# Kernel tuning notes

Hardware: AMD Instinct MI355X
Metric: run time of the kernel (lower is better)

The kernel has to match this reference:

```python
import jax, jax.numpy as jnp
import numpy as np

V, E, H2, B, T, OUT = 50000, 300, 512, 32, 512, 256
H = H2 // 2  # hidden per direction


def _rand_mask(key, lengths, n_true):
    # exactly n_true True positions per row, all within the valid prefix [0, len)
    t = jnp.arange(T)[None, :]
    r = jax.random.uniform(key, (B, T)) + (t >= lengths[:, None]) * 10.0
    idx = jnp.argsort(r, axis=1)[:, :n_true]
    mask = jnp.zeros((B, T), dtype=bool)
    return mask.at[jnp.arange(B)[:, None], idx].set(True)


def setup_inputs() -> dict:
    key = jax.random.key(0)
    ks = jax.random.split(key, 12)
    inputs = jax.random.randint(ks[0], (B, T), 0, V)
    lengths = jnp.sort(jax.random.randint(ks[1], (B,), OUT, T + 1))[::-1]
    lengths = lengths.at[0].set(T)  # max length == padded length
    fmask = _rand_mask(ks[2], lengths, OUT)
    bmask = _rand_mask(ks[3], lengths, OUT)
    emb_scale = np.sqrt(3.0 / E).astype(np.float32)
    emb = jax.random.uniform(ks[4], (V, E), minval=-emb_scale, maxval=emb_scale, dtype=jnp.float32)
    k = 1.0 / np.sqrt(H).astype(np.float32)
    def u(kk, shape):
        return jax.random.uniform(kk, shape, minval=-k, maxval=k, dtype=jnp.float32)
    return {
        'inputs': inputs, 'seq_length': lengths, 'fmask': fmask, 'bmask': bmask,
        'out_seq_length': OUT, 'emb': emb,
        'W_ih_f': u(ks[5], (4 * H, E)), 'W_hh_f': u(ks[6], (4 * H, H)),
        'b_ih_f': u(ks[7], (4 * H,)), 'b_hh_f': u(ks[8], (4 * H,)),
        'W_ih_b': u(ks[9], (4 * H, E)), 'W_hh_b': u(ks[10], (4 * H, H)),
        'b_ih_b': u(ks[11], (4 * H,)), 'b_hh_b': u(ks[7], (4 * H,)),
    }


def run_lstm(xe, W_ih, W_hh, b_ih, b_hh):
    # PyTorch LSTM cell, gate order i,f,g,o. xe: (B,T,E) -> (B,T,H)
    xg = jnp.einsum('bte,ge->btg', xe, W_ih) + (b_ih + b_hh)
    def step(carry, xg_t):
        h, c = carry
        g = xg_t + h @ W_hh.T
        i, f, gg, o = jnp.split(g, 4, axis=-1)
        c = jax.nn.sigmoid(f) * c + jax.nn.sigmoid(i) * jnp.tanh(gg)
        h = jax.nn.sigmoid(o) * jnp.tanh(c)
        return (h, c), h
    h0 = jnp.zeros((xe.shape[0], W_hh.shape[1]), xe.dtype)
    _, hs = jax.lax.scan(step, (h0, h0), xg.transpose(1, 0, 2))
    return hs.transpose(1, 0, 2)


def select_masked(x, mask, out_len):
    # masked_select row-major order == indices of True in increasing t
    idx = jnp.argsort(jnp.logical_not(mask), axis=1, stable=True)[:, :out_len]
    return jnp.take_along_axis(x, idx[:, :, None], axis=1)


def reference(inputs, seq_length, fmask, bmask, out_seq_length, emb,
              W_ih_f, W_hh_f, b_ih_f, b_hh_f, W_ih_b, W_hh_b, b_ih_b, b_hh_b):
    t = jnp.arange(inputs.shape[1])[None, :]          # (1,T)
    valid = t < seq_length[:, None]                   # (B,T)
    # forward direction (dropout is identity at inference)
    f_out = run_lstm(emb[inputs], W_ih_f, W_hh_f, b_ih_f, b_hh_f)
    f_out = f_out * valid[..., None]                  # pad_packed zeros beyond len
    fsel = select_masked(f_out, fmask, out_seq_length)
    # per-batch sequence reversal of valid prefix (padding stays in place)
    rev_idx = jnp.where(valid, seq_length[:, None] - 1 - t, t)
    rinputs = jnp.take_along_axis(inputs, rev_idx, axis=1)
    b_out = run_lstm(emb[rinputs], W_ih_b, W_hh_b, b_ih_b, b_hh_b)
    b_out = b_out * valid[..., None]
    bsel = select_masked(b_out, bmask, out_seq_length)
    # re-reverse selected backward outputs per batch
    k = jnp.minimum(seq_length, out_seq_length)[:, None]
    t2 = jnp.arange(out_seq_length)[None, :]
    idx2 = jnp.where(t2 < k, out_seq_length - 1 - t2, t2 - k)
    bsel = jnp.take_along_axis(bsel, idx2[:, :, None], axis=1)
    return jnp.concatenate([fsel, bsel], axis=2)      # (B,out_seq,2H)
```

## Files before the change

### kernel.cpp

```cpp
#include <hip/hip_runtime.h>
#include <hip/hip_bf16.h>

#define B_   32
#define T_   512
#define E_   300
#define H_   256
#define OUT_ 256
#define ECH  100
#define GROWP 293

typedef unsigned long long u64;

__global__ __launch_bounds__(64) void slots_kernel(
    const unsigned char* __restrict__ fm, const unsigned char* __restrict__ bm,
    int* __restrict__ fslot, int* __restrict__ bpos)
{
    __shared__ unsigned char fL[B_ * T_];
    __shared__ unsigned char bL[B_ * T_];
    const int tid = threadIdx.x;

    const unsigned int* fw = (const unsigned int*)fm;
    int cnt = 0;
    for (int i = tid; i < 128; i += 64) {
        unsigned int v = fw[i];
        cnt += ((v & 0xFFu) != 0) + ((v & 0xFF00u) != 0)
             + ((v & 0xFF0000u) != 0) + ((v >> 24) != 0);
    }
#pragma unroll
    for (int off = 32; off; off >>= 1) cnt += __shfl_down(cnt, off, 64);
    bool isbool = __shfl(cnt, 0, 64) > 128;

    if (isbool) {
        for (int i = tid; i < B_ * T_ / 4; i += 64) {
            ((unsigned int*)fL)[i] = ((const unsigned int*)fm)[i];
            ((unsigned int*)bL)[i] = ((const unsigned int*)bm)[i];
        }
    } else {
        const unsigned int* bw = (const unsigned int*)bm;
        for (int i = tid; i < B_ * T_; i += 64) {
            fL[i] = fw[i] != 0;
            bL[i] = bw[i] != 0;
        }
    }
    __syncthreads();

    if (tid < B_) {
        int jf = 0, jb = 0;
        for (int t = 0; t < T_; ++t) {
            bool f = fL[tid * T_ + t] != 0;
            bool g = bL[tid * T_ + t] != 0;
            fslot[tid * T_ + t] = f ? (jf++) : -1;
            bpos [tid * T_ + t] = g ? (OUT_ - 1 - (jb++)) : -1;
        }
    }
}

__global__ __launch_bounds__(256) void xg_gemm(
    const int* __restrict__ inputs, const int* __restrict__ seqlen,
    const float* __restrict__ emb,
    const float* __restrict__ Wihf, const float* __restrict__ Wihb,
    const float* __restrict__ bihf, const float* __restrict__ bhhf,
    const float* __restrict__ bihb, const float* __restrict__ bhhb,
    float* __restrict__ xg, int t0, int TcMax)
{
    const int tg   = blockIdx.y;
    const int dir  = blockIdx.z;
    const int rblk = blockIdx.x * 64;
    const int tid  = threadIdx.x;

    __shared__ float eL[4][B_][ECH];
    __shared__ int   tokS[4][B_];

    if (tid < 128) {
        int t4 = tid >> 5, b = tid & 31;
        int t = t0 + tg * 4 + t4;
        int L = seqlen[b];
        int tt = t;
        if (dir) tt = (t < L) ? (L - 1 - t) : t;
        tokS[t4][b] = inputs[b * T_ + tt];
    }

    const float* W = dir ? Wihb : Wihf;
    const int b  = tid & 31;
    const int r8 = tid >> 5;

    float acc[4][8];
#pragma unroll
    for (int t4 = 0; t4 < 4; ++t4)
#pragma unroll
        for (int m = 0; m < 8; ++m) acc[t4][m] = 0.f;

    for (int ec = 0; ec < 3; ++ec) {
        __syncthreads();
        for (int idx = tid; idx < 3200; idx += 256) {
            int q  = idx % 25;
            int bb = (idx / 25) & 31;
            int t4 = idx / (25 * 32);
            const float* erow = emb + (size_t)tokS[t4][bb] * E_ + ec * ECH;
            *(float4*)&eL[t4][bb][q * 4] = *(const float4*)(erow + q * 4);
        }
        __syncthreads();

        for (int e4 = 0; e4 < 25; ++e4) {
            float4 w4[8];
#pragma unroll
            for (int m = 0; m < 8; ++m)
                w4[m] = *(const float4*)(W + (size_t)(rblk + r8 + m * 8) * E_
                                         + ec * ECH + e4 * 4);
#pragma unroll
            for (int t4 = 0; t4 < 4; ++t4) {
                float4 h4 = *(const float4*)&eL[t4][b][e4 * 4];
#pragma unroll
                for (int m = 0; m < 8; ++m)
                    acc[t4][m] += h4.x * w4[m].x + h4.y * w4[m].y
                                + h4.z * w4[m].z + h4.w * w4[m].w;
            }
        }
    }

    const float* bi = dir ? bihb : bihf;
    const float* bh = dir ? bhhb : bhhf;
#pragma unroll
    for (int t4 = 0; t4 < 4; ++t4) {
        float* outp = xg + (size_t)(dir * TcMax + tg * 4 + t4) * (1024 * B_);
#pragma unroll
        for (int m = 0; m < 8; ++m) {
            int row = rblk + r8 + m * 8;
            outp[(size_t)row * B_ + b] = acc[t4][m] + bi[row] + bh[row];
        }
    }
}

__global__ __launch_bounds__(512, 2) void fused_lstm(
    const int* __restrict__ inputs, const int* __restrict__ seqlen,
    const float* __restrict__ emb,
    const float* __restrict__ Wihf, const float* __restrict__ Whhf,
    const float* __restrict__ bihf, const float* __restrict__ bhhf,
    const float* __restrict__ Wihb, const float* __restrict__ Whhb,
    const float* __restrict__ bihb, const float* __restrict__ bhhb,
    const int* __restrict__ fslot, const int* __restrict__ bpos,
    float* __restrict__ hbuf, float* __restrict__ cbuf,
    int* __restrict__ barr, int* __restrict__ xgcnt,
    float* __restrict__ xg, float* __restrict__ out,
    int t0, int Tc, int fused)
{
    const int wg  = blockIdx.x;
    const int tid = threadIdx.x;
    __shared__ __align__(16) float smem[13824];

    if (wg >= 128) {
        float* eL   = smem;
        int*   tokS = (int*)(smem + 12800);
        const int hw = wg - 128;

        for (int j = hw; j < 2048; j += 128) {
            const int tg  = j >> 4;
            const int dir = (j >> 3) & 1;
            const int rp  = j & 7;
            const int rblk = (rp * 2 + (tid >> 8)) * 64;

            if (tid < 128) {
                int t4 = tid >> 5, b = tid & 31;
                int t = tg * 4 + t4;
                int L = seqlen[b];
                int tt = t;
                if (dir) tt = (t < L) ? (L - 1 - t) : t;
                tokS[t4 * B_ + b] = inputs[b * T_ + tt];
            }

            const float* W  = dir ? Wihb : Wihf;
            const int ltid = tid & 255;
            const int b  = ltid & 31;
            const int r8 = ltid >> 5;

            float acc[4][8];
#pragma unroll
            for (int t4 = 0; t4 < 4; ++t4)
#pragma unroll
                for (int m = 0; m < 8; ++m) acc[t4][m] = 0.f;

            for (int ec = 0; ec < 3; ++ec) {
                __syncthreads();
                for (int idx = tid; idx < 3200; idx += 512) {
                    int q  = idx % 25;
                    int bb = (idx / 25) & 31;
                    int t4 = idx / (25 * 32);
                    const float* erow = emb + (size_t)tokS[t4 * B_ + bb] * E_ + ec * ECH;
                    *(float4*)&eL[(t4 * B_ + bb) * ECH + q * 4] = *(const float4*)(erow + q * 4);
                }
                __syncthreads();

                for (int e4 = 0; e4 < 25; ++e4) {
                    float4 w4[8];
#pragma unroll
                    for (int m = 0; m < 8; ++m)
                        w4[m] = *(const float4*)(W + (size_t)(rblk + r8 + m * 8) * E_
                                                 + ec * ECH + e4 * 4);
#pragma unroll
                    for (int t4 = 0; t4 < 4; ++t4) {
                        float4 h4 = *(const float4*)&eL[(t4 * B_ + b) * ECH + e4 * 4];
#pragma unroll
                        for (int m = 0; m < 8; ++m)
                            acc[t4][m] += h4.x * w4[m].x + h4.y * w4[m].y
                                        + h4.z * w4[m].z + h4.w * w4[m].w;
                    }
                }
            }

            const float* bi = dir ? bihb : bihf;
            const float* bh = dir ? bhhb : bhhf;
#pragma unroll
            for (int t4 = 0; t4 < 4; ++t4) {
                float* outp = xg + (size_t)(dir * 512 + tg * 4 + t4) * (1024 * B_);
#pragma unroll
                for (int m = 0; m < 8; ++m) {
                    int row = rblk + r8 + m * 8;
                    __hip_atomic_store(&outp[(size_t)row * B_ + b],
                                       acc[t4][m] + bi[row] + bh[row],
                                       __ATOMIC_RELAXED, __HIP_MEMORY_SCOPE_AGENT);
                }
            }
            __syncthreads();
            if (tid == 0)
                __hip_atomic_fetch_add(&xgcnt[dir * 128 + tg], 1,
                                       __ATOMIC_RELAXED, __HIP_MEMORY_SCOPE_AGENT);
        }
        return;
    }

    float* hP   = smem;
    float* gbuf = smem + 8704;
    int*   sL   = (int*)(smem + 8704 + 4688);

    const int dir = wg >> 6;
    const int wgd = wg & 63;
    const int u0  = wgd * 4;

    const int rg  = tid & 3;
    const int bgr = (tid >> 2) & 7;
    const int kq  = tid >> 5;

    const float* Whh = dir ? Whhb : Whhf;

    float w[4][16];
#pragma unroll
    for (int r = 0; r < 4; ++r) {
        const float* wr = Whh + (size_t)(rg * H_ + u0 + r) * H_ + kq * 16;
#pragma unroll
        for (int q = 0; q < 4; ++q) {
            float4 v = *(const float4*)(wr + q * 4);
            w[r][q * 4 + 0] = v.x; w[r][q * 4 + 1] = v.y;
            w[r][q * 4 + 2] = v.z; w[r][q * 4 + 3] = v.w;
        }
    }
    if (tid < B_) sL[tid] = seqlen[tid];
    __syncthreads();

    const int ul = (tid >> 5) & 3, bb = tid & 31;
    float c_reg = 0.f;
    if (t0 > 0 && tid < 128)
        c_reg = cbuf[(size_t)(dir * 64 + wgd) * 128 + ul * 32 + bb];

    if (fused) {
        if (tid == 0) {
            const int* xc = xgcnt + dir * 128 + (t0 >> 2);
            while (__hip_atomic_load(xc, __ATOMIC_RELAXED,
                                     __HIP_MEMORY_SCOPE_AGENT) < 8)
                __builtin_amdgcn_s_sleep(1);
        }
        __syncthreads();
    }
    float xgv0 = 0.f, xgv1 = 0.f, xgv2 = 0.f, xgv3 = 0.f;
    if (tid < 128) {
        const float* xp = xg + (size_t)(dir * Tc) * 32768 + (u0 + ul) * 32 + bb;
        xgv0 = __hip_atomic_load(xp, __ATOMIC_RELAXED, __HIP_MEMORY_SCOPE_AGENT);
        xgv1 = __hip_atomic_load(xp + 256 * 32, __ATOMIC_RELAXED, __HIP_MEMORY_SCOPE_AGENT);
        xgv2 = __hip_atomic_load(xp + 512 * 32, __ATOMIC_RELAXED, __HIP_MEMORY_SCOPE_AGENT);
        xgv3 = __hip_atomic_load(xp + 768 * 32, __ATOMIC_RELAXED, __HIP_MEMORY_SCOPE_AGENT);
    }

    int* myflag = barr + dir * 64 + wgd;

    for (int tc = 0; tc < Tc; ++tc) {
        const int t = t0 + tc;

        if (tc > 0) {
            if (tid < 64) {
                const int* fp = barr + dir * 64 + tid;
                const int gneed = (fused && tc + 1 < Tc) ? ((t0 + tc + 1) >> 2) : -1;
                const int* xc = xgcnt + dir * 128 + (gneed < 0 ? 0 : gneed);
                for (;;) {
                    bool ok = __hip_atomic_load(fp, __ATOMIC_RELAXED,
                                                __HIP_MEMORY_SCOPE_AGENT) >= tc;
                    if (gneed >= 0 && tid == 0)
                        ok = ok && (__hip_atomic_load(xc, __ATOMIC_RELAXED,
                                                      __HIP_MEMORY_SCOPE_AGENT) >= 8);
                    if (__all(ok)) break;
                    __builtin_amdgcn_s_sleep(1);
                }
            }
            __syncthreads();
        }

        float xgn0 = 0.f, xgn1 = 0.f, xgn2 = 0.f, xgn3 = 0.f;
        if (tc + 1 < Tc && tid < 128) {
            const float* xp = xg + (size_t)(dir * Tc + tc + 1) * 32768 + (u0 + ul) * 32 + bb;
            xgn0 = __hip_atomic_load(xp, __ATOMIC_RELAXED, __HIP_MEMORY_SCOPE_AGENT);
            xgn1 = __hip_atomic_load(xp + 256 * 32, __ATOMIC_RELAXED, __HIP_MEMORY_SCOPE_AGENT);
            xgn2 = __hip_atomic_load(xp + 512 * 32, __ATOMIC_RELAXED, __HIP_MEMORY_SCOPE_AGENT);
            xgn3 = __hip_atomic_load(xp + 768 * 32, __ATOMIC_RELAXED, __HIP_MEMORY_SCOPE_AGENT);
        }

        u64 hr[8];
        if (t > 0) {
            const u64* hp64 = (const u64*)(hbuf +
                (size_t)(dir * 2 + ((t - 1) & 1)) * (64 * 32 * 4));
#pragma unroll
            for (int i = 0; i < 8; ++i)
                hr[i] = __hip_atomic_load(hp64 + tid + 512 * i, __ATOMIC_RELAXED,
                                          __HIP_MEMORY_SCOPE_AGENT);
#pragma unroll
            for (int i = 0; i < 8; ++i) {
                int g = tid + 512 * i;
                int f4 = g >> 1, jp = g & 1;
                int k4 = f4 >> 5, b = f4 & 31;
                int base = ((k4 >> 2) * 8 + (b >> 2)) * 68 + (k4 & 3) * 16 + (b & 3);
                union { u64 u; float f[2]; } cv; cv.u = hr[i];
                hP[base + 8 * jp]     = cv.f[0];
                hP[base + 8 * jp + 4] = cv.f[1];
            }
        }
        __syncthreads();

        float acc[4][4];
#pragma unroll
        for (int r = 0; r < 4; ++r)
#pragma unroll
            for (int bi = 0; bi < 4; ++bi) acc[r][bi] = 0.f;

        if (t > 0) {
            const float* hblk = &hP[(kq * 8 + bgr) * 68];
#pragma unroll
            for (int kk = 0; kk < 16; ++kk) {
                float4 h4 = *(const float4*)(hblk + kk * 4);
#pragma unroll
                for (int r = 0; r < 4; ++r) {
                    acc[r][0] += w[r][kk] * h4.x;
                    acc[r][1] += w[r][kk] * h4.y;
                    acc[r][2] += w[r][kk] * h4.z;
                    acc[r][3] += w[r][kk] * h4.w;
                }
            }
        }

#pragma unroll
        for (int r = 0; r < 4; ++r)
#pragma unroll
            for (int bi = 0; bi < 4; ++bi)
                acc[r][bi] += __shfl_xor(acc[r][bi], 32, 64);

        if (((tid >> 5) & 1) == 0) {
            const int kq2 = kq >> 1;
#pragma unroll
            for (int r = 0; r < 4; ++r)
#pragma unroll
                for (int bi = 0; bi < 4; ++bi)
                    gbuf[(r * 4 + rg) * GROWP + (bgr * 4 + bi) * 9 + kq2] = acc[r][bi];
        }
        __syncthreads();

        if (tid < 128) {
            const int u = u0 + ul;
            float hnew;
            if (t < sL[bb]) {
                float gi = xgv0, gf = xgv1, gg = xgv2, go = xgv3;
#pragma unroll
                for (int q = 0; q < 8; ++q) {
                    gi += gbuf[(ul * 4 + 0) * GROWP + bb * 9 + q];
                    gf += gbuf[(ul * 4 + 1) * GROWP + bb * 9 + q];
                    gg += gbuf[(ul * 4 + 2) * GROWP + bb * 9 + q];
                    go += gbuf[(ul * 4 + 3) * GROWP + bb * 9 + q];
                }
                float si = 1.f / (1.f + expf(-gi));
                float sf = 1.f / (1.f + expf(-gf));
                float so = 1.f / (1.f + expf(-go));
                c_reg = sf * c_reg + si * tanhf(gg);
                hnew  = so * tanhf(c_reg);
                if (dir == 0) {
                    int j = fslot[bb * T_ + t];
                    if (j >= 0)
                        __hip_atomic_store(&out[((size_t)bb * OUT_ + j) * 512 + u],
                                           hnew, __ATOMIC_RELAXED,
                                           __HIP_MEMORY_SCOPE_AGENT);
                } else {
                    int p = bpos[bb * T_ + t];
                    if (p >= 0)
                        __hip_atomic_store(&out[((size_t)bb * OUT_ + p) * 512 + 256 + u],
                                           hnew, __ATOMIC_RELAXED,
                                           __HIP_MEMORY_SCOPE_AGENT);
                }
            } else {
                hnew = hP[((u >> 4) * 8 + (bb >> 2)) * 68 + (u & 15) * 4 + (bb & 3)];
            }
            float* hn = hbuf + (size_t)(dir * 2 + (t & 1)) * (64 * 32 * 4);
            __hip_atomic_store(&hn[(wgd * 32 + bb) * 4 + ul], hnew,
                               __ATOMIC_RELAXED, __HIP_MEMORY_SCOPE_AGENT);
        }
        xgv0 = xgn0; xgv1 = xgn1; xgv2 = xgn2; xgv3 = xgn3;
        __syncthreads();

        if (tc + 1 < Tc && tid == 0)
            __hip_atomic_store(myflag, tc + 1, __ATOMIC_RELAXED,
                               __HIP_MEMORY_SCOPE_AGENT);
    }

    if (tid < 128)
        cbuf[(size_t)(dir * 64 + wgd) * 128 + ul * 32 + bb] = c_reg;
}

extern "C" void kernel_launch(void* const* d_in, const int* in_sizes, int n_in,
                              void* d_out, int out_size, void* d_ws, size_t ws_size,
                              hipStream_t stream) {
    const int*           inputs = (const int*)d_in[0];
    const int*           seqlen = (const int*)d_in[1];
    const unsigned char* fm     = (const unsigned char*)d_in[2];
    const unsigned char* bm     = (const unsigned char*)d_in[3];
    const float* emb  = (const float*)d_in[5];
    const float* Wihf = (const float*)d_in[6];
    const float* Whhf = (const float*)d_in[7];
    const float* bihf = (const float*)d_in[8];
    const float* bhhf = (const float*)d_in[9];
    const float* Wihb = (const float*)d_in[10];
    const float* Whhb = (const float*)d_in[11];
    const float* bihb = (const float*)d_in[12];
    const float* bhhb = (const float*)d_in[13];
    float* out = (float*)d_out;

    char* ws = (char*)d_ws;
    int*   fslot = (int*)(ws);
    int*   bpos  = (int*)(ws + 65536);
    float* hbuf  = (float*)(ws + 131072);
    float* cbuf  = (float*)(ws + 262144);
    int*   barr  = (int*)(ws + 327680);
    int*   xgcnt = (int*)(ws + 328192);
    float* xg    = (float*)(ws + 393216);
    (void)in_sizes; (void)n_in; (void)out_size;

    size_t avail = (ws_size > 393216) ? ws_size - 393216 : 0;
    int Tc = 4;
    for (int c = 512; c >= 4; c >>= 1)
        if ((size_t)c * 262144 <= avail) { Tc = c; break; }

    slots_kernel<<<1, 64, 0, stream>>>(fm, bm, fslot, bpos);

    if (Tc == 512) {
        (void)hipMemsetAsync(barr, 0, 512 + 1024, stream);
        fused_lstm<<<256, 512, 0, stream>>>(
            inputs, seqlen, emb, Wihf, Whhf, bihf, bhhf,
            Wihb, Whhb, bihb, bhhb, fslot, bpos,
            hbuf, cbuf, barr, xgcnt, xg, out, 0, 512, 1);
    } else {
        for (int t0 = 0; t0 < T_; t0 += Tc) {
            dim3 g(16, Tc / 4, 2);
            xg_gemm<<<g, 256, 0, stream>>>(inputs, seqlen, emb, Wihf, Wihb,
                                           bihf, bhhf, bihb, bhhb, xg, t0, Tc);
            (void)hipMemsetAsync(barr, 0, 512 + 1024, stream);
            fused_lstm<<<128, 512, 0, stream>>>(
                inputs, seqlen, emb, Wihf, Whhf, bihf, bhhf,
                Wihb, Whhb, bihb, bhhb, fslot, bpos,
                hbuf, cbuf, barr, xgcnt, xg, out, t0, Tc, 0);
        }
    }
}
```

Measured before the change: 2.087 ms.

## Poll barrier flags in every wave, relayout h exchange, defer output stores

```diff
diff --git a/kernel.cpp b/kernel.cpp
--- a/kernel.cpp
+++ b/kernel.cpp
@@ -239,6 +239,8 @@
     const int rg  = tid & 3;
     const int bgr = (tid >> 2) & 7;
     const int kq  = tid >> 5;
+    const int wv  = tid >> 6;
+    const int lane = tid & 63;
 
     const float* Whh = dir ? Whhb : Whhf;
 
@@ -285,21 +287,18 @@
         const int t = t0 + tc;
 
         if (tc > 0) {
-            if (tid < 64) {
-                const int* fp = barr + dir * 64 + tid;
-                const int gneed = (fused && tc + 1 < Tc) ? ((t0 + tc + 1) >> 2) : -1;
-                const int* xc = xgcnt + dir * 128 + (gneed < 0 ? 0 : gneed);
-                for (;;) {
-                    bool ok = __hip_atomic_load(fp, __ATOMIC_RELAXED,
-                                                __HIP_MEMORY_SCOPE_AGENT) >= tc;
-                    if (gneed >= 0 && tid == 0)
-                        ok = ok && (__hip_atomic_load(xc, __ATOMIC_RELAXED,
-                                                      __HIP_MEMORY_SCOPE_AGENT) >= 8);
-                    if (__all(ok)) break;
-                    __builtin_amdgcn_s_sleep(1);
-                }
-            }
-            __syncthreads();
+            const int* fp = barr + dir * 64 + wv + 8 * (lane & 7);
+            const int gneed = (fused && wv < 2 && tc + 1 < Tc) ? ((t0 + tc + 1) >> 2) : -1;
+            const int* xc = xgcnt + dir * 128 + (gneed < 0 ? 0 : gneed);
+            for (;;) {
+                bool ok = __hip_atomic_load(fp, __ATOMIC_RELAXED,
+                                            __HIP_MEMORY_SCOPE_AGENT) >= tc;
+                if (gneed >= 0)
+                    ok = ok && (__hip_atomic_load(xc, __ATOMIC_RELAXED,
+                                                  __HIP_MEMORY_SCOPE_AGENT) >= 8);
+                if (__all(ok)) break;
+                __builtin_amdgcn_s_sleep(1);
+            }
         }
 
         float xgn0 = 0.f, xgn1 = 0.f, xgn2 = 0.f, xgn3 = 0.f;
@@ -311,23 +310,21 @@
             xgn3 = __hip_atomic_load(xp + 768 * 32, __ATOMIC_RELAXED, __HIP_MEMORY_SCOPE_AGENT);
         }
 
-        u64 hr[8];
         if (t > 0) {
             const u64* hp64 = (const u64*)(hbuf +
-                (size_t)(dir * 2 + ((t - 1) & 1)) * (64 * 32 * 4));
+                (size_t)(dir * 2 + ((t - 1) & 1)) * 8192);
+            u64 hr[8];
 #pragma unroll
             for (int i = 0; i < 8; ++i)
                 hr[i] = __hip_atomic_load(hp64 + tid + 512 * i, __ATOMIC_RELAXED,
                                           __HIP_MEMORY_SCOPE_AGENT);
 #pragma unroll
             for (int i = 0; i < 8; ++i) {
-                int g = tid + 512 * i;
-                int f4 = g >> 1, jp = g & 1;
-                int k4 = f4 >> 5, b = f4 & 31;
-                int base = ((k4 >> 2) * 8 + (b >> 2)) * 68 + (k4 & 3) * 16 + (b & 3);
-                union { u64 u; float f[2]; } cv; cv.u = hr[i];
-                hP[base + 8 * jp]     = cv.f[0];
-                hP[base + 8 * jp + 4] = cv.f[1];
+                int j = tid + 512 * i;
+                int k  = (j >> 6) * 4 + ((j >> 4) & 3);
+                int b0 = (j & 15) * 2;
+                int addr = ((k >> 4) * 8 + (b0 >> 2)) * 68 + (k & 15) * 4 + (b0 & 3);
+                *(u64*)&hP[addr] = hr[i];
             }
         }
         __syncthreads();
@@ -369,9 +366,10 @@
         }
         __syncthreads();
 
+        float hnew = 0.f;
+        float* oaddr = nullptr;
         if (tid < 128) {
             const int u = u0 + ul;
-            float hnew;
             if (t < sL[bb]) {
                 float gi = xgv0, gf = xgv1, gg = xgv2, go = xgv3;
 #pragma unroll
@@ -388,22 +386,16 @@
                 hnew  = so * tanhf(c_reg);
                 if (dir == 0) {
                     int j = fslot[bb * T_ + t];
-                    if (j >= 0)
-                        __hip_atomic_store(&out[((size_t)bb * OUT_ + j) * 512 + u],
-                                           hnew, __ATOMIC_RELAXED,
-                                           __HIP_MEMORY_SCOPE_AGENT);
+                    if (j >= 0) oaddr = &out[((size_t)bb * OUT_ + j) * 512 + u];
                 } else {
                     int p = bpos[bb * T_ + t];
-                    if (p >= 0)
-                        __hip_atomic_store(&out[((size_t)bb * OUT_ + p) * 512 + 256 + u],
-                                           hnew, __ATOMIC_RELAXED,
-                                           __HIP_MEMORY_SCOPE_AGENT);
+                    if (p >= 0) oaddr = &out[((size_t)bb * OUT_ + p) * 512 + 256 + u];
                 }
             } else {
                 hnew = hP[((u >> 4) * 8 + (bb >> 2)) * 68 + (u & 15) * 4 + (bb & 3)];
             }
-            float* hn = hbuf + (size_t)(dir * 2 + (t & 1)) * (64 * 32 * 4);
-            __hip_atomic_store(&hn[(wgd * 32 + bb) * 4 + ul], hnew,
+            float* hn = hbuf + (size_t)(dir * 2 + (t & 1)) * 8192;
+            __hip_atomic_store(&hn[wgd * 128 + tid], hnew,
                                __ATOMIC_RELAXED, __HIP_MEMORY_SCOPE_AGENT);
         }
         xgv0 = xgn0; xgv1 = xgn1; xgv2 = xgn2; xgv3 = xgn3;
@@ -411,6 +403,9 @@
 
         if (tc + 1 < Tc && tid == 0)
             __hip_atomic_store(myflag, tc + 1, __ATOMIC_RELAXED,
+                               __HIP_MEMORY_SCOPE_AGENT);
+        if (oaddr)
+            __hip_atomic_store(oaddr, hnew, __ATOMIC_RELAXED,
                                __HIP_MEMORY_SCOPE_AGENT);
     }
 
```

Measured after the change: 2.039 ms. 1.02x faster.
